# Performance work log

Hardware: AMD Instinct MI355X
Metric: run time of the kernel (lower is better)

The kernel has to match this reference:

```python
import jax, jax.numpy as jnp
import numpy as np

SIGMA_INIT = 1000.0


def setup_inputs() -> dict:
    key = jax.random.key(0)
    k1, k2, k3 = jax.random.split(key, 3)
    B, M, D, S = 1024, 209, 12288, 2
    input_data = jax.random.normal(k1, (B, D), dtype=jnp.float32)
    center = jax.random.normal(k2, (M, D), dtype=jnp.float32)
    sigma = SIGMA_INIT * jnp.ones((M,), dtype=jnp.float32)
    W = 50.0 * jax.random.normal(k3, (S, M), dtype=jnp.float32)
    b = jnp.zeros((S,), dtype=jnp.float32)
    return {"input_data": input_data, "center": center, "sigma": sigma, "W": W, "b": b}


def reference(input_data, center, sigma, W, b):
    # Euclidean distance ||x_i - c_j|| via GEMM expansion (avoids [B,M,D] diff tensor)
    x2 = jnp.sum(input_data * input_data, axis=1, keepdims=True)        # [B,1]
    c2 = jnp.sum(center * center, axis=1)[None, :]                      # [1,M]
    d2 = x2 + c2 - 2.0 * (input_data @ center.T)                        # [B,M]
    dist = jnp.sqrt(jnp.maximum(d2, 0.0))
    # Note: original divides the (non-squared) norm by sigma^2, then exp(-.)
    radial = jnp.exp(-dist / (sigma * sigma)[None, :])                  # [B,M]
    return radial @ W.T + b                                             # [B,S]
```

## Files before the change

kernel.cpp:

```cpp
#include <hip/hip_runtime.h>
#include <hip/hip_bf16.h>
#include <stdint.h>

#define B_SZ 1024
#define M_SZ 209
#define MPAD 224
#define D_SZ 12288
#define KC   32
#define KCH  384
#define BK   128
#define NIT  (KCH / BK)
#define NB   32
#define BT   32
#define NCT  7
#define SROW 224
#define SLROW (KC * SROW)

#define CBF_OFF  0u
#define XXP_OFF  (MPAD * D_SZ)
#define CCP_OFF  (XXP_OFF + B_SZ * KC * 4)
#define SLAB_OFF (CCP_OFF + MPAD * 2 * 4)

typedef __attribute__((ext_vector_type(8))) short short8;
typedef __attribute__((ext_vector_type(4))) float floatx4;

__device__ __forceinline__ uint32_t pk8x4(const float4& v) {
    int d = __builtin_amdgcn_cvt_pk_fp8_f32(v.x, v.y, 0, false);
    d     = __builtin_amdgcn_cvt_pk_fp8_f32(v.z, v.w, d, true);
    return (uint32_t)d;
}

__device__ __forceinline__ float bfbits2f(unsigned short u) {
    union { uint32_t u; float f; } cv;
    cv.u = ((uint32_t)u) << 16;
    return cv.f;
}

__device__ __forceinline__ void gload_lds16(const void* g, void* l) {
    __builtin_amdgcn_global_load_lds(
        (const __attribute__((address_space(1))) void*)g,
        (__attribute__((address_space(3))) void*)l, 16, 0, 0);
}

__global__ __launch_bounds__(256) void rbf_prep(
    const float* __restrict__ c, uint8_t* __restrict__ cf8,
    float* __restrict__ ccp)
{
    __shared__ float red[4];
    const int j = blockIdx.x >> 1, h = blockIdx.x & 1;
    const int t = threadIdx.x;
    const int base = h * (D_SZ / 2);
    uint8_t* dst = cf8 + (size_t)j * D_SZ + base;
    float s = 0.f;
    if (j < M_SZ) {
        const float* src = c + (size_t)j * D_SZ + base;
        for (int i = t * 8; i < D_SZ / 2; i += 2048) {
            float4 v0 = *(const float4*)(src + i);
            float4 v1 = *(const float4*)(src + i + 4);
            s += v0.x*v0.x + v0.y*v0.y + v0.z*v0.z + v0.w*v0.w
               + v1.x*v1.x + v1.y*v1.y + v1.z*v1.z + v1.w*v1.w;
            uint2 w = { pk8x4(v0), pk8x4(v1) };
            *(uint2*)(dst + i) = w;
        }
    } else {
        uint2 zz = {0u, 0u};
        for (int i = t * 8; i < D_SZ / 2; i += 2048) *(uint2*)(dst + i) = zz;
    }
#pragma unroll
    for (int off = 32; off > 0; off >>= 1) s += __shfl_down(s, off);
    if ((t & 63) == 0) red[t >> 6] = s;
    __syncthreads();
    if (t == 0) ccp[j * 2 + h] = red[0] + red[1] + red[2] + red[3];
}

__global__ __launch_bounds__(256, 4) void rbf_main(
    const float* __restrict__ x, const uint8_t* __restrict__ cf8,
    __hip_bfloat16* __restrict__ slab, float* __restrict__ xxp)
{
    __shared__ uint8_t sx[BT * BK];
    __shared__ uint8_t sc[MPAD * BK];

    const int t    = threadIdx.x;
    const int k    = blockIdx.x;
    const int b    = blockIdx.y;
    const int wave = t >> 6, lane = t & 63;
    const int quad = lane >> 4, mrow = lane & 15;
    const int qh = quad >> 1, ql = quad & 1;
    const int s2 = (mrow >> 1) & 7;
    const int rt  = wave & 1;
    const int cth = wave >> 1;

    floatx4 acc[NCT];
    const floatx4 z4 = {0.f, 0.f, 0.f, 0.f};
#pragma unroll
    for (int i = 0; i < NCT; ++i) acc[i] = z4;

    const int oE = (((lane & 7) ^ (lane >> 4)) & 7) * 16;
    const int oO = ((((lane & 7) ^ (lane >> 4)) ^ 4) & 7) * 16;
    const uint8_t* cpbE = cf8 + (size_t)(lane >> 3) * D_SZ + (size_t)k * KCH + oE;
    const uint8_t* cpbO = cf8 + (size_t)(lane >> 3) * D_SZ + (size_t)k * KCH + oO;

#pragma unroll
    for (int jj = 0; jj < 7; ++jj) {
        const int cr = wave * 7 + jj;
        const uint8_t* p = ((cr & 1) ? cpbO : cpbE) + (size_t)cr * 8 * D_SZ;
        gload_lds16(p, &sc[cr * 1024]);
    }

    const int xr = t >> 3;
    const int xc = t & 7;
    const float* xp = x + (size_t)(b * BT + xr) * D_SZ + (size_t)k * KCH + xc * 16;

    uint4 xw[NIT];
    float sxx = 0.f;
#pragma unroll
    for (int it = 0; it < NIT; ++it) {
        float4 v0 = *(const float4*)(xp + it * BK + 0);
        float4 v1 = *(const float4*)(xp + it * BK + 4);
        float4 v2 = *(const float4*)(xp + it * BK + 8);
        float4 v3 = *(const float4*)(xp + it * BK + 12);
        sxx += v0.x*v0.x + v0.y*v0.y + v0.z*v0.z + v0.w*v0.w
             + v1.x*v1.x + v1.y*v1.y + v1.z*v1.z + v1.w*v1.w
             + v2.x*v2.x + v2.y*v2.y + v2.z*v2.z + v2.w*v2.w
             + v3.x*v3.x + v3.y*v3.y + v3.z*v3.z + v3.w*v3.w;
        xw[it] = make_uint4(pk8x4(v0), pk8x4(v1), pk8x4(v2), pk8x4(v3));
    }
    uint8_t* sxw = &sx[xr * BK + ((xc ^ ((xr >> 1) & 7)) & 7) * 16];

    int boff[4];
#pragma unroll
    for (int ks = 0; ks < 4; ++ks)
        boff[ks] = (((ks * 2 + qh) ^ s2) & 7) * 16 + ql * 8;
    const uint8_t* abase = &sx[(rt * 16 + mrow) * BK];
    const uint8_t* bbase = &sc[(cth * 7 * 16 + mrow) * BK];

    for (int it = 0; it < NIT; ++it) {
        *(uint4*)sxw = xw[it];
        __syncthreads();
#pragma unroll
        for (int ks = 0; ks < 4; ++ks) {
            const long a = *(const long*)(abase + boff[ks]);
#pragma unroll
            for (int ct = 0; ct < NCT; ++ct) {
                const long bv = *(const long*)(bbase + ct * 16 * BK + boff[ks]);
                acc[ct] = __builtin_amdgcn_mfma_f32_16x16x32_fp8_fp8(a, bv, acc[ct], 0, 0, 0);
            }
        }
        __syncthreads();
        if (it + 1 < NIT) {
#pragma unroll
            for (int jj = 0; jj < 7; ++jj) {
                const int cr = wave * 7 + jj;
                const uint8_t* p = ((cr & 1) ? cpbO : cpbE)
                                 + (size_t)cr * 8 * D_SZ + (it + 1) * BK;
                gload_lds16(p, &sc[cr * 1024]);
            }
        }
    }

    __hip_bfloat16* sd = slab + (size_t)k * SROW;
    const int gi0 = b * BT + rt * 16 + quad * 4;
#pragma unroll
    for (int ct = 0; ct < NCT; ++ct) {
        const int gj = (cth * 7 + ct) * 16 + mrow;
#pragma unroll
        for (int rg = 0; rg < 4; ++rg)
            sd[(size_t)(gi0 + rg) * SLROW + gj] = __float2bfloat16(acc[ct][rg]);
    }

    sxx += __shfl_down(sxx, 4);
    sxx += __shfl_down(sxx, 2);
    sxx += __shfl_down(sxx, 1);
    if ((t & 7) == 0) xxp[(size_t)(b * BT + xr) * KC + k] = sxx;
}

__global__ __launch_bounds__(256) void rbf_fin(
    const __hip_bfloat16* __restrict__ slab, const float* __restrict__ xxp,
    const float* __restrict__ ccp, const float* __restrict__ sigma,
    const float* __restrict__ W, const float* __restrict__ bias,
    float* __restrict__ out)
{
    __shared__ float jpart[MPAD * 9];
    __shared__ float jtot[MPAD];
    __shared__ float xsh;

    const int t = threadIdx.x;
    const int i = blockIdx.x;

    if (t < 64) {
        float xv = (t < KC) ? xxp[(size_t)i * KC + t] : 0.f;
#pragma unroll
        for (int off = 32; off > 0; off >>= 1) xv += __shfl_down(xv, off);
        if (t == 0) xsh = xv;
    }

    const int o = t % 28, g = t / 28;
    if (t < 252) {
        const unsigned short* sp = (const unsigned short*)slab
                                 + (size_t)i * SLROW + o * 8;
        float s8[8] = {0.f,0.f,0.f,0.f,0.f,0.f,0.f,0.f};
        for (int kk = g; kk < KC; kk += 9) {
            short8 v = *(const short8*)(sp + kk * SROW);
#pragma unroll
            for (int e = 0; e < 8; ++e) s8[e] += bfbits2f((unsigned short)v[e]);
        }
#pragma unroll
        for (int e = 0; e < 8; ++e) jpart[(o * 8 + e) * 9 + g] = s8[e];
    }
    __syncthreads();

    if (t < MPAD) {
        float d = 0.f;
#pragma unroll
        for (int g2 = 0; g2 < 9; ++g2) d += jpart[t * 9 + g2];
        jtot[t] = d;
    }
    __syncthreads();

    if (t < 64) {
        const float xxi = xsh;
        float a0 = 0.f, a1 = 0.f;
        for (int j = t; j < M_SZ; j += 64) {
            const float ccj = ccp[j * 2] + ccp[j * 2 + 1];
            float d2 = fmaxf(xxi + ccj - 2.f * jtot[j], 0.f);
            float sg = sigma[j];
            float rad = __expf(-sqrtf(d2) / (sg * sg));
            a0 += rad * W[j];
            a1 += rad * W[M_SZ + j];
        }
#pragma unroll
        for (int off = 32; off > 0; off >>= 1) {
            a0 += __shfl_down(a0, off);
            a1 += __shfl_down(a1, off);
        }
        if (t == 0) {
            out[i * 2 + 0] = a0 + bias[0];
            out[i * 2 + 1] = a1 + bias[1];
        }
    }
}

extern "C" void kernel_launch(void* const* d_in, const int* in_sizes, int n_in,
                              void* d_out, int out_size, void* d_ws, size_t ws_size,
                              hipStream_t stream)
{
    const float* x     = (const float*)d_in[0];
    const float* c     = (const float*)d_in[1];
    const float* sigma = (const float*)d_in[2];
    const float* W     = (const float*)d_in[3];
    const float* bias  = (const float*)d_in[4];
    float* out = (float*)d_out;

    char* ws = (char*)d_ws;
    uint8_t*        cf8  = (uint8_t*)(ws + CBF_OFF);
    float*          xxp  = (float*)(ws + XXP_OFF);
    float*          ccp  = (float*)(ws + CCP_OFF);
    __hip_bfloat16* slab = (__hip_bfloat16*)(ws + SLAB_OFF);

    rbf_prep<<<MPAD * 2, 256, 0, stream>>>(c, cf8, ccp);
    rbf_main<<<dim3(KC, NB), 256, 0, stream>>>(x, cf8, slab, xxp);
    rbf_fin<<<B_SZ, 256, 0, stream>>>(slab, xxp, ccp, sigma, W, bias, out);
}
```

Measured before the change: 111.4 us.

## Halve split-K chunks and store partial GEMM slabs as fp8 instead of bf16

Cuts the split-K factor from 32 to 16, so each block loops over twice as many D elements, and fully unrolls that loop. Partial dot products are now written to the workspace slab as fp8 bytes rather than bf16, which shrinks slab traffic for both the main and final kernels. The occupancy hint drops from 4 to 2 blocks per SM to allow more registers. Storing the partial sums in fp8 adds substantial rounding error to values that are later combined into distances. The grid also shrinks to 512 blocks, which lowers parallelism.

```diff
diff --git a/kernel.cpp b/kernel.cpp
--- a/kernel.cpp
+++ b/kernel.cpp
@@ -6,8 +6,8 @@
 #define M_SZ 209
 #define MPAD 224
 #define D_SZ 12288
-#define KC   32
-#define KCH  384
+#define KC   16
+#define KCH  768
 #define BK   128
 #define NIT  (KCH / BK)
 #define NB   32
@@ -28,12 +28,6 @@
     int d = __builtin_amdgcn_cvt_pk_fp8_f32(v.x, v.y, 0, false);
     d     = __builtin_amdgcn_cvt_pk_fp8_f32(v.z, v.w, d, true);
     return (uint32_t)d;
-}
-
-__device__ __forceinline__ float bfbits2f(unsigned short u) {
-    union { uint32_t u; float f; } cv;
-    cv.u = ((uint32_t)u) << 16;
-    return cv.f;
 }
 
 __device__ __forceinline__ void gload_lds16(const void* g, void* l) {
@@ -73,9 +67,9 @@
     if (t == 0) ccp[j * 2 + h] = red[0] + red[1] + red[2] + red[3];
 }
 
-__global__ __launch_bounds__(256, 4) void rbf_main(
+__global__ __launch_bounds__(256, 2) void rbf_main(
     const float* __restrict__ x, const uint8_t* __restrict__ cf8,
-    __hip_bfloat16* __restrict__ slab, float* __restrict__ xxp)
+    uint8_t* __restrict__ slab, float* __restrict__ xxp)
 {
     __shared__ uint8_t sx[BT * BK];
     __shared__ uint8_t sc[MPAD * BK];
@@ -134,6 +128,7 @@
     const uint8_t* abase = &sx[(rt * 16 + mrow) * BK];
     const uint8_t* bbase = &sc[(cth * 7 * 16 + mrow) * BK];
 
+#pragma unroll
     for (int it = 0; it < NIT; ++it) {
         *(uint4*)sxw = xw[it];
         __syncthreads();
@@ -158,14 +153,18 @@
         }
     }
 
-    __hip_bfloat16* sd = slab + (size_t)k * SROW;
+    uint8_t* sd = slab + (size_t)k * SROW;
     const int gi0 = b * BT + rt * 16 + quad * 4;
 #pragma unroll
     for (int ct = 0; ct < NCT; ++ct) {
         const int gj = (cth * 7 + ct) * 16 + mrow;
-#pragma unroll
-        for (int rg = 0; rg < 4; ++rg)
-            sd[(size_t)(gi0 + rg) * SLROW + gj] = __float2bfloat16(acc[ct][rg]);
+        const int p01 = __builtin_amdgcn_cvt_pk_fp8_f32(acc[ct][0], acc[ct][1], 0, false);
+        const int p23 = __builtin_amdgcn_cvt_pk_fp8_f32(acc[ct][2], acc[ct][3], 0, false);
+        uint8_t* wb = sd + (size_t)gi0 * SLROW + gj;
+        wb[0]                   = (uint8_t)(p01 & 0xff);
+        wb[SLROW]               = (uint8_t)((p01 >> 8) & 0xff);
+        wb[2 * (size_t)SLROW]   = (uint8_t)(p23 & 0xff);
+        wb[3 * (size_t)SLROW]   = (uint8_t)((p23 >> 8) & 0xff);
     }
 
     sxx += __shfl_down(sxx, 4);
@@ -175,7 +174,7 @@
 }
 
 __global__ __launch_bounds__(256) void rbf_fin(
-    const __hip_bfloat16* __restrict__ slab, const float* __restrict__ xxp,
+    const uint8_t* __restrict__ slab, const float* __restrict__ xxp,
     const float* __restrict__ ccp, const float* __restrict__ sigma,
     const float* __restrict__ W, const float* __restrict__ bias,
     float* __restrict__ out)
@@ -196,13 +195,18 @@
 
     const int o = t % 28, g = t / 28;
     if (t < 252) {
-        const unsigned short* sp = (const unsigned short*)slab
-                                 + (size_t)i * SLROW + o * 8;
+        const uint8_t* sp = slab + (size_t)i * SLROW + o * 8;
         float s8[8] = {0.f,0.f,0.f,0.f,0.f,0.f,0.f,0.f};
         for (int kk = g; kk < KC; kk += 9) {
-            short8 v = *(const short8*)(sp + kk * SROW);
-#pragma unroll
-            for (int e = 0; e < 8; ++e) s8[e] += bfbits2f((unsigned short)v[e]);
+            uint2 v = *(const uint2*)(sp + (size_t)kk * SROW);
+            s8[0] += __builtin_amdgcn_cvt_f32_fp8((int)v.x, 0);
+            s8[1] += __builtin_amdgcn_cvt_f32_fp8((int)v.x, 1);
+            s8[2] += __builtin_amdgcn_cvt_f32_fp8((int)v.x, 2);
+            s8[3] += __builtin_amdgcn_cvt_f32_fp8((int)v.x, 3);
+            s8[4] += __builtin_amdgcn_cvt_f32_fp8((int)v.y, 0);
+            s8[5] += __builtin_amdgcn_cvt_f32_fp8((int)v.y, 1);
+            s8[6] += __builtin_amdgcn_cvt_f32_fp8((int)v.y, 2);
+            s8[7] += __builtin_amdgcn_cvt_f32_fp8((int)v.y, 3);
         }
 #pragma unroll
         for (int e = 0; e < 8; ++e) jpart[(o * 8 + e) * 9 + g] = s8[e];
@@ -252,10 +256,10 @@
     float* out = (float*)d_out;
 
     char* ws = (char*)d_ws;
-    uint8_t*        cf8  = (uint8_t*)(ws + CBF_OFF);
-    float*          xxp  = (float*)(ws + XXP_OFF);
-    float*          ccp  = (float*)(ws + CCP_OFF);
-    __hip_bfloat16* slab = (__hip_bfloat16*)(ws + SLAB_OFF);
+    uint8_t* cf8  = (uint8_t*)(ws + CBF_OFF);
+    float*   xxp  = (float*)(ws + XXP_OFF);
+    float*   ccp  = (float*)(ws + CCP_OFF);
+    uint8_t* slab = (uint8_t*)(ws + SLAB_OFF);
 
     rbf_prep<<<MPAD * 2, 256, 0, stream>>>(c, cf8, ccp);
     rbf_main<<<dim3(KC, NB), 256, 0, stream>>>(x, cf8, slab, xxp);
```

After: 110.4 us. About the same (-0.9%).
